# Optimization experiments

Measured on AMD Instinct MI355X. Metric: run time of the kernel, lower is better.

The kernel has to match this reference:

```python
import jax, jax.numpy as jnp
import numpy as np

E = 7       # number of experts (len(expert_details))
K = 2       # top-k routing
CAP = 3072  # per-expert capacity ~ ceil(T*K/E * 1.25)
D = 1024    # d_model
H = 4096    # d_ff = 4*d_model
T = 8192    # tokens (B=2, S=4096)


def setup_inputs() -> dict:
    key = jax.random.key(0)
    k1, k2, k3, k4 = jax.random.split(key, 4)
    x = jax.random.normal(k1, (T, D), jnp.float32)
    Wg = jax.random.normal(k2, (D, E), jnp.float32) * 0.02
    W1 = jax.random.normal(k3, (E, D, H), jnp.float32) * 0.02
    W2 = jax.random.normal(k4, (E, H, D), jnp.float32) * 0.02
    return {"x": x, "Wg": Wg, "W1": W1, "W2": W2}


def reference(x, Wg, W1, W2):
    Tn, Dn = x.shape
    # --- router ---
    gates = jax.nn.softmax(x @ Wg, axis=-1)          # [T, E]
    topw, topi = jax.lax.top_k(gates, K)             # [T, K]
    topw = topw / jnp.sum(topw, axis=-1, keepdims=True)
    flat_e = topi.reshape(-1)                        # [T*K] expert ids (int)
    flat_w = topw.reshape(-1)                        # [T*K] combine weights
    # --- position within each expert (priority = token order) ---
    onehot = jax.nn.one_hot(flat_e, E, dtype=jnp.int32)           # [T*K, E]
    pos = jnp.sum(jnp.cumsum(onehot, axis=0) * onehot, axis=-1) - 1  # [T*K]
    keep = pos < CAP
    slot = jnp.where(keep, pos, CAP)  # overflow tokens go to pad slot CAP
    # --- dispatch: scatter tokens into [E, CAP, D] buffer ---
    x_rep = jnp.repeat(x, K, axis=0)                               # [T*K, D]
    buf = jnp.zeros((E, CAP + 1, Dn), x.dtype).at[flat_e, slot].set(x_rep)[:, :CAP]
    # --- grouped expert FFN (grouped GEMMs) ---
    h = jax.nn.gelu(jnp.einsum('ecd,edh->ech', buf, W1))
    y = jnp.einsum('ech,ehd->ecd', h, W2)                          # [E, CAP, D]
    # --- combine: gather back and weight ---
    y_pad = jnp.concatenate([y, jnp.zeros((E, 1, Dn), y.dtype)], axis=1)
    out_slots = y_pad[flat_e, slot] * (flat_w * keep.astype(flat_w.dtype))[:, None]
    return out_slots.reshape(Tn, K, Dn).sum(axis=1)                # [T, D]
```

## Files before the change

### kernel.cpp

```cpp
#include <hip/hip_runtime.h>
#include <stdint.h>


#define NEXP 7
#define KTOP 2
#define CAP 3072
#define DM 1024
#define HF 4096
#define TT 8192

typedef __bf16 bf16x8 __attribute__((ext_vector_type(8)));
typedef float f32x4 __attribute__((ext_vector_type(4)));

__device__ __forceinline__ unsigned short f2bf(float v) {
  union { float f; unsigned u; } a; a.f = v;
  unsigned r = a.u + 0x7FFFu + ((a.u >> 16) & 1u);
  return (unsigned short)(r >> 16);
}
__device__ __forceinline__ float bf2f(unsigned short h) {
  union { unsigned u; float f; } a; a.u = ((unsigned)h) << 16; return a.f;
}
__device__ __forceinline__ float gelu_t(float v) {
  float u = 0.7978845608028654f * (v + 0.044715f * v * v * v);
  float ex = __expf(2.0f * u);
  float th = 1.0f - 2.0f / (ex + 1.0f);
  return 0.5f * v * (1.0f + th);
}
__device__ __forceinline__ void gl2lds16(const void* g, void* l) {
  __builtin_amdgcn_global_load_lds(
      (const __attribute__((address_space(1))) unsigned int*)g,
      (__attribute__((address_space(3))) unsigned int*)l, 16, 0, 0);
}

__global__ void init_counts(int* counts) {
  if (threadIdx.x < NEXP) counts[threadIdx.x] = 0;
}

__global__ void router_kernel(const float* __restrict__ x, const float* __restrict__ Wg,
                              int* __restrict__ counts, int* __restrict__ flatE,
                              int* __restrict__ flatSlot, int* __restrict__ tokOfSlot,
                              float* __restrict__ wOfSlot) {
  int wave = threadIdx.x >> 6, lane = threadIdx.x & 63;
  int t = blockIdx.x * 4 + wave;
  double acc[NEXP];
#pragma unroll
  for (int e = 0; e < NEXP; ++e) acc[e] = 0.0;
  const float* xr = x + (long)t * DM;
  for (int j = 0; j < DM / 64; ++j) {
    int d = j * 64 + lane;
    double xv = (double)xr[d];
#pragma unroll
    for (int e = 0; e < NEXP; ++e) acc[e] += xv * (double)Wg[d * NEXP + e];
  }
#pragma unroll
  for (int e = 0; e < NEXP; ++e) {
#pragma unroll
    for (int off = 32; off > 0; off >>= 1) acc[e] += __shfl_down(acc[e], off);
  }
  if (lane == 0) {
    int i1 = 0; double l1 = acc[0];
    for (int e2 = 1; e2 < NEXP; ++e2) if (acc[e2] > l1) { l1 = acc[e2]; i1 = e2; }
    int i2 = -1; double l2 = -1e300;
    for (int e2 = 0; e2 < NEXP; ++e2) if (e2 != i1 && acc[e2] > l2) { l2 = acc[e2]; i2 = e2; }
    float w1 = (float)(1.0 / (1.0 + exp(l2 - l1)));
    float w2 = 1.0f - w1;
    int fi0 = t * 2, fi1 = t * 2 + 1;
    int p0 = atomicAdd(&counts[i1], 1);
    flatE[fi0] = i1; flatSlot[fi0] = (p0 < CAP) ? p0 : CAP;
    if (p0 < CAP) { tokOfSlot[i1 * CAP + p0] = fi0; wOfSlot[i1 * CAP + p0] = w1; }
    int p1 = atomicAdd(&counts[i2], 1);
    flatE[fi1] = i2; flatSlot[fi1] = (p1 < CAP) ? p1 : CAP;
    if (p1 < CAP) { tokOfSlot[i2 * CAP + p1] = fi1; wOfSlot[i2 * CAP + p1] = w2; }
  }
}

__global__ void transcvt(const float* __restrict__ in, unsigned short* __restrict__ out,
                         int R, int C) {
  __shared__ float tile[64][65];
  long base = (long)blockIdx.z * (long)R * (long)C;
  const float* inp = in + base;
  unsigned short* outp = out + base;
  int c0 = blockIdx.x * 64, r0 = blockIdx.y * 64;
  int lx = threadIdx.x & 63, ly = threadIdx.x >> 6;
#pragma unroll
  for (int i = 0; i < 16; ++i) {
    int r = ly + i * 4;
    tile[r][lx] = inp[(long)(r0 + r) * C + c0 + lx];
  }
  __syncthreads();
#pragma unroll
  for (int i = 0; i < 16; ++i) {
    int c = ly + i * 4;
    outp[(long)(c0 + c) * R + r0 + lx] = f2bf(tile[lx][c]);
  }
}

__global__ void scatter_x(const float* __restrict__ x, const int* __restrict__ flatE,
                          const int* __restrict__ flatSlot, unsigned short* __restrict__ xb) {
  int fi = blockIdx.x;
  int s = flatSlot[fi];
  if (s >= CAP) return;
  int e = flatE[fi];
  const float4* xr = (const float4*)(x + (long)(fi >> 1) * DM);
  float4 v = xr[threadIdx.x];
  ushort4 o; o.x = f2bf(v.x); o.y = f2bf(v.y); o.z = f2bf(v.z); o.w = f2bf(v.w);
  ((ushort4*)(xb + ((long)e * CAP + s) * DM))[threadIdx.x] = o;
}

template <int EPI>
__global__ __launch_bounds__(512, 2) void gemm256(
    const unsigned short* __restrict__ A, const unsigned short* __restrict__ Bt,
    void* __restrict__ Cout, const int* __restrict__ counts,
    const int* __restrict__ tokOfSlot, const float* __restrict__ wOfSlot,
    int LD, int klen, int N, int kspl, long aexps, long cexps) {
  __shared__ __align__(16) unsigned short sAb[2][16384];
  __shared__ __align__(16) unsigned short sBb[2][16384];
  int e = blockIdx.z / kspl, ks = blockIdx.z % kspl;
  int mcnt = counts[e]; mcnt = mcnt < CAP ? mcnt : CAP;
  int m0 = blockIdx.y * 256;
  if (m0 >= mcnt) return;
  int n0 = blockIdx.x * 256;
  long kstart = (long)ks * klen;

  const unsigned short* Ae = A + (long)e * aexps;
  const unsigned short* Be = Bt + (long)e * (long)N * LD;

  int tid = threadIdx.x;
  int lane = tid & 63, wave = tid >> 6;
  int wr = wave >> 2, wc = wave & 3;
  int lm = lane & 15, quad = lane >> 4;

  int srow = tid >> 3;
  int scol = ((lane & 7) ^ (lane >> 3)) << 3;
  const unsigned short* As = Ae + (long)(m0 + srow) * LD + kstart + scol;
  const unsigned short* Bs = Be + (long)(n0 + srow) * LD + kstart + scol;

  int abase = (wr * 128 + lm) * 64;
  int bbase = (wc * 64 + lm) * 64;
  int cx0 = (quad ^ (lm & 7)) << 3;
  int cx1 = ((quad + 4) ^ (lm & 7)) << 3;

  f32x4 acc[8][4];
#pragma unroll
  for (int i = 0; i < 8; ++i)
#pragma unroll
    for (int j = 0; j < 4; ++j) acc[i][j] = f32x4{0.f, 0.f, 0.f, 0.f};

  int NT = klen >> 6, NI = NT >> 1;

#define STA(buf, kt, half) do { \
    int _kt = (kt) < NT ? (kt) : (NT - 1); \
    gl2lds16(As + (long)_kt * 64 + (long)((half) * 2) * 64 * LD, \
             &sAb[buf][(half) * 8192 + tid * 8]); \
    gl2lds16(As + (long)_kt * 64 + (long)((half) * 2 + 1) * 64 * LD, \
             &sAb[buf][(half) * 8192 + 4096 + tid * 8]); \
  } while (0)
#define STB(buf, kt, half) do { \
    int _kt = (kt) < NT ? (kt) : (NT - 1); \
    gl2lds16(Bs + (long)_kt * 64 + (long)((half) * 2) * 64 * LD, \
             &sBb[buf][(half) * 8192 + tid * 8]); \
    gl2lds16(Bs + (long)_kt * 64 + (long)((half) * 2 + 1) * 64 * LD, \
             &sBb[buf][(half) * 8192 + 4096 + tid * 8]); \
  } while (0)

  bf16x8 bF[4][2];

#define PHASE(buf, mi0, RB, STAGE, VM) do { \
    bf16x8 a00 = *(const bf16x8*)&sAb[buf][abase + (mi0) * 1024 + cx0]; \
    bf16x8 a01 = *(const bf16x8*)&sAb[buf][abase + (mi0) * 1024 + cx1]; \
    bf16x8 a10 = *(const bf16x8*)&sAb[buf][abase + (mi0) * 1024 + 1024 + cx0]; \
    bf16x8 a11 = *(const bf16x8*)&sAb[buf][abase + (mi0) * 1024 + 1024 + cx1]; \
    if (RB) { \
      _Pragma("unroll") \
      for (int ni = 0; ni < 4; ++ni) { \
        bF[ni][0] = *(const bf16x8*)&sBb[buf][bbase + ni * 1024 + cx0]; \
        bF[ni][1] = *(const bf16x8*)&sBb[buf][bbase + ni * 1024 + cx1]; \
      } \
    } \
    STAGE; \
    __builtin_amdgcn_s_barrier(); \
    asm volatile("s_waitcnt lgkmcnt(0)" ::: "memory"); \
    __builtin_amdgcn_sched_barrier(0); \
    __builtin_amdgcn_s_setprio(1); \
    _Pragma("unroll") \
    for (int ni = 0; ni < 4; ++ni) { \
      acc[mi0][ni]     = __builtin_amdgcn_mfma_f32_16x16x32_bf16(a00, bF[ni][0], acc[mi0][ni], 0, 0, 0); \
      acc[mi0][ni]     = __builtin_amdgcn_mfma_f32_16x16x32_bf16(a01, bF[ni][1], acc[mi0][ni], 0, 0, 0); \
      acc[mi0 + 1][ni] = __builtin_amdgcn_mfma_f32_16x16x32_bf16(a10, bF[ni][0], acc[mi0 + 1][ni], 0, 0, 0); \
      acc[mi0 + 1][ni] = __builtin_amdgcn_mfma_f32_16x16x32_bf16(a11, bF[ni][1], acc[mi0 + 1][ni], 0, 0, 0); \
    } \
    __builtin_amdgcn_s_setprio(0); \
    VM; \
    __builtin_amdgcn_s_barrier(); \
  } while (0)

  STA(0, 0, 0); STA(0, 0, 1); STB(0, 0, 0); STB(0, 0, 1);
  STB(1, 1, 0); STB(1, 1, 1);
  asm volatile("s_waitcnt vmcnt(4)" ::: "memory");
  __builtin_amdgcn_s_barrier();

  for (int t = 0; t < NI; ++t) {
    int k0 = 2 * t, k1 = 2 * t + 1;
    PHASE(0, 0, 1, STA(1, k1, 0), (void)0);
    PHASE(0, 2, 0, STA(1, k1, 1), (void)0);
    PHASE(0, 4, 0, STB(0, k0 + 2, 0), (void)0);
    PHASE(0, 6, 0, STB(0, k0 + 2, 1),
          asm volatile("s_waitcnt vmcnt(4)" ::: "memory"));
    PHASE(1, 0, 1, STA(0, k0 + 2, 0), (void)0);
    PHASE(1, 2, 0, STA(0, k0 + 2, 1), (void)0);
    PHASE(1, 4, 0, STB(1, k1 + 2, 0), (void)0);
    PHASE(1, 6, 0, STB(1, k1 + 2, 1),
          asm volatile("s_waitcnt vmcnt(4)" ::: "memory"));
  }
  asm volatile("s_waitcnt vmcnt(0)" ::: "memory");
#undef PHASE
#undef STA
#undef STB

  if (EPI == 0) {
    unsigned short* Ce = (unsigned short*)Cout + (long)e * cexps;
#pragma unroll
    for (int mi = 0; mi < 8; ++mi) {
      int mb = m0 + wr * 128 + mi * 16 + quad * 4;
#pragma unroll
      for (int r = 0; r < 4; ++r) {
        int m = mb + r;
        if (m < mcnt) {
#pragma unroll
          for (int ni = 0; ni < 4; ++ni) {
            int n = n0 + wc * 64 + ni * 16 + lm;
            Ce[(long)m * N + n] = f2bf(gelu_t(acc[mi][ni][r]));
          }
        }
      }
    }
  } else {
    unsigned short* Y = (unsigned short*)Cout + (long)ks * ((long)TT * KTOP * DM);
#pragma unroll
    for (int mi = 0; mi < 8; ++mi) {
      int mb = m0 + wr * 128 + mi * 16 + quad * 4;
#pragma unroll
      for (int r = 0; r < 4; ++r) {
        int m = mb + r;
        if (m < mcnt) {
          int fi = tokOfSlot[e * CAP + m];
          float w = wOfSlot[e * CAP + m];
#pragma unroll
          for (int ni = 0; ni < 4; ++ni) {
            int n = n0 + wc * 64 + ni * 16 + lm;
            Y[(long)fi * N + n] = f2bf(w * acc[mi][ni][r]);
          }
        }
      }
    }
  }
}

template <int EPI>
__global__ __launch_bounds__(256, 2) void gemm_bt(
    const unsigned short* __restrict__ A, const unsigned short* __restrict__ Bt,
    void* __restrict__ Cout, const int* __restrict__ counts,
    const int* __restrict__ tokOfSlot, const float* __restrict__ wOfSlot,
    int K, int N, int eoff, long aexps, long cexps) {
  __shared__ unsigned short sA[128 * 32];
  __shared__ unsigned short sB[128 * 32];
  int e = eoff + blockIdx.z;
  int mcnt = counts[e]; mcnt = mcnt < CAP ? mcnt : CAP;
  int m0 = blockIdx.y * 128;
  if (m0 >= mcnt) return;
  int n0 = blockIdx.x * 128;
  const unsigned short* Ae = A + (long)blockIdx.z * aexps;
  const unsigned short* Be = Bt + (long)e * (long)N * (long)K;

  int tid = threadIdx.x;
  int lane = tid & 63, wave = tid >> 6;
  int lm = lane & 15, quad = lane >> 4;
  int wm = (wave & 1) * 64, wn = (wave >> 1) * 64;

  int ra = tid >> 2;
  int ca = (tid & 3) * 8;
  const unsigned short* Ab0 = Ae + (long)(m0 + ra) * K + ca;
  const unsigned short* Ab1 = Ae + (long)(m0 + 64 + ra) * K + ca;
  const unsigned short* Bb0 = Be + (long)(n0 + ra) * K + ca;
  const unsigned short* Bb1 = Be + (long)(n0 + 64 + ra) * K + ca;
  unsigned short* sAp0 = &sA[tid * 8];
  unsigned short* sAp1 = &sA[(tid + 256) * 8];
  unsigned short* sBp0 = &sB[tid * 8];
  unsigned short* sBp1 = &sB[(tid + 256) * 8];

  f32x4 acc[4][4];
#pragma unroll
  for (int i = 0; i < 4; ++i)
#pragma unroll
    for (int j = 0; j < 4; ++j) acc[i][j] = f32x4{0.f, 0.f, 0.f, 0.f};

  for (int k0 = 0; k0 < K; k0 += 32) {
    gl2lds16(Ab0 + k0, sAp0);
    gl2lds16(Ab1 + k0, sAp1);
    gl2lds16(Bb0 + k0, sBp0);
    gl2lds16(Bb1 + k0, sBp1);
    __syncthreads();
    bf16x8 aF[4], bFf[4];
#pragma unroll
    for (int mi = 0; mi < 4; ++mi)
      aF[mi] = *(const bf16x8*)&sA[(wm + mi * 16 + lm) * 32 + quad * 8];
#pragma unroll
    for (int ni = 0; ni < 4; ++ni)
      bFf[ni] = *(const bf16x8*)&sB[(wn + ni * 16 + lm) * 32 + quad * 8];
#pragma unroll
    for (int mi = 0; mi < 4; ++mi)
#pragma unroll
      for (int ni = 0; ni < 4; ++ni)
        acc[mi][ni] = __builtin_amdgcn_mfma_f32_16x16x32_bf16(aF[mi], bFf[ni], acc[mi][ni], 0, 0, 0);
    __syncthreads();
  }

  if (EPI == 0) {
    unsigned short* Ce = (unsigned short*)Cout + (long)blockIdx.z * cexps;
#pragma unroll
    for (int mi = 0; mi < 4; ++mi) {
      int mb = m0 + wm + mi * 16 + quad * 4;
#pragma unroll
      for (int r = 0; r < 4; ++r) {
        int m = mb + r;
        if (m < mcnt) {
#pragma unroll
          for (int ni = 0; ni < 4; ++ni) {
            int n = n0 + wn + ni * 16 + lm;
            Ce[(long)m * N + n] = f2bf(gelu_t(acc[mi][ni][r]));
          }
        }
      }
    }
  } else {
    unsigned short* Y = (unsigned short*)Cout;
#pragma unroll
    for (int mi = 0; mi < 4; ++mi) {
      int mb = m0 + wm + mi * 16 + quad * 4;
#pragma unroll
      for (int r = 0; r < 4; ++r) {
        int m = mb + r;
        if (m < mcnt) {
          int fi = tokOfSlot[e * CAP + m];
          float w = wOfSlot[e * CAP + m];
#pragma unroll
          for (int ni = 0; ni < 4; ++ni) {
            int n = n0 + wn + ni * 16 + lm;
            Y[(long)fi * N + n] = f2bf(w * acc[mi][ni][r]);
          }
        }
      }
    }
  }
}

__global__ void combine_k2(const unsigned short* __restrict__ yflat,
                           const int* __restrict__ flatSlot, float* __restrict__ out) {
  int t = blockIdx.x;
  bool k0 = flatSlot[2 * t] < CAP, k1 = flatSlot[2 * t + 1] < CAP;
  const long S = (long)TT * KTOP * DM;
  const ushort4* y00 = (const ushort4*)(yflat + (long)(2 * t) * DM);
  const ushort4* y01 = (const ushort4*)(yflat + S + (long)(2 * t) * DM);
  const ushort4* y10 = (const ushort4*)(yflat + (long)(2 * t + 1) * DM);
  const ushort4* y11 = (const ushort4*)(yflat + S + (long)(2 * t + 1) * DM);
  ushort4 a = y00[threadIdx.x], a2 = y01[threadIdx.x];
  ushort4 b = y10[threadIdx.x], b2 = y11[threadIdx.x];
  float4 r;
  r.x = (k0 ? bf2f(a.x) + bf2f(a2.x) : 0.f) + (k1 ? bf2f(b.x) + bf2f(b2.x) : 0.f);
  r.y = (k0 ? bf2f(a.y) + bf2f(a2.y) : 0.f) + (k1 ? bf2f(b.y) + bf2f(b2.y) : 0.f);
  r.z = (k0 ? bf2f(a.z) + bf2f(a2.z) : 0.f) + (k1 ? bf2f(b.z) + bf2f(b2.z) : 0.f);
  r.w = (k0 ? bf2f(a.w) + bf2f(a2.w) : 0.f) + (k1 ? bf2f(b.w) + bf2f(b2.w) : 0.f);
  ((float4*)(out + (long)t * DM))[threadIdx.x] = r;
}

__global__ void combine_k(const unsigned short* __restrict__ yflat,
                          const int* __restrict__ flatSlot, float* __restrict__ out) {
  int t = blockIdx.x;
  bool k0 = flatSlot[2 * t] < CAP, k1 = flatSlot[2 * t + 1] < CAP;
  const ushort4* y0 = (const ushort4*)(yflat + (long)(2 * t) * DM);
  const ushort4* y1 = (const ushort4*)(yflat + (long)(2 * t + 1) * DM);
  ushort4 a = y0[threadIdx.x], b = y1[threadIdx.x];
  float4 r;
  r.x = (k0 ? bf2f(a.x) : 0.f) + (k1 ? bf2f(b.x) : 0.f);
  r.y = (k0 ? bf2f(a.y) : 0.f) + (k1 ? bf2f(b.y) : 0.f);
  r.z = (k0 ? bf2f(a.z) : 0.f) + (k1 ? bf2f(b.z) : 0.f);
  r.w = (k0 ? bf2f(a.w) : 0.f) + (k1 ? bf2f(b.w) : 0.f);
  ((float4*)(out + (long)t * DM))[threadIdx.x] = r;
}

extern "C" void kernel_launch(void* const* d_in, const int* in_sizes, int n_in,
                              void* d_out, int out_size, void* d_ws, size_t ws_size,
                              hipStream_t stream) {
  const float* x  = (const float*)d_in[0];
  const float* Wg = (const float*)d_in[1];
  const float* W1 = (const float*)d_in[2];
  const float* W2 = (const float*)d_in[3];
  float* out = (float*)d_out;

  char* ws = (char*)d_ws;
  size_t off = 0;
  auto alloc = [&](size_t b) { void* p = ws + off; off = (off + b + 255) & ~(size_t)255; return p; };
  int* counts            = (int*)alloc(NEXP * 4);
  int* flatE             = (int*)alloc((size_t)TT * KTOP * 4);
  int* flatSlot          = (int*)alloc((size_t)TT * KTOP * 4);
  int* tokOfSlot         = (int*)alloc((size_t)NEXP * CAP * 4);
  float* wOfSlot         = (float*)alloc((size_t)NEXP * CAP * 4);
  unsigned short* Wb1    = (unsigned short*)alloc((size_t)NEXP * DM * HF * 2);
  unsigned short* Wb2    = (unsigned short*)alloc((size_t)NEXP * DM * HF * 2);
  unsigned short* xb     = (unsigned short*)alloc((size_t)NEXP * CAP * DM * 2);
  unsigned short* yflat  = (unsigned short*)alloc((size_t)2 * TT * KTOP * DM * 2);
  size_t hbA = (size_t)NEXP * CAP * HF * 2;
  size_t hbB = (size_t)CAP * HF * 2;
  int planA = (off + hbA) <= ws_size;
  unsigned short* hb = (unsigned short*)alloc(planA ? hbA : hbB);

  init_counts<<<1, 64, 0, stream>>>(counts);
  router_kernel<<<TT / 4, 256, 0, stream>>>(x, Wg, counts, flatE, flatSlot, tokOfSlot, wOfSlot);
  transcvt<<<dim3(HF / 64, DM / 64, NEXP), 256, 0, stream>>>(W1, Wb1, DM, HF);
  transcvt<<<dim3(DM / 64, HF / 64, NEXP), 256, 0, stream>>>(W2, Wb2, HF, DM);
  scatter_x<<<TT * KTOP, 256, 0, stream>>>(x, flatE, flatSlot, xb);

  if (planA) {
    gemm256<0><<<dim3(HF / 256, CAP / 256, NEXP), 512, 0, stream>>>(
        xb, Wb1, hb, counts, tokOfSlot, wOfSlot, DM, DM, HF, 1,
        (long)CAP * DM, (long)CAP * HF);
    gemm256<1><<<dim3(DM / 256, CAP / 256, NEXP * 2), 512, 0, stream>>>(
        hb, Wb2, yflat, counts, tokOfSlot, wOfSlot, HF, HF / 2, DM, 2,
        (long)CAP * HF, 0);
    combine_k2<<<TT, 256, 0, stream>>>(yflat, flatSlot, out);
  } else {
    for (int e = 0; e < NEXP; ++e) {
      gemm_bt<0><<<dim3(HF / 128, CAP / 128, 1), 256, 0, stream>>>(
          xb + (size_t)e * CAP * DM, Wb1, hb, counts, tokOfSlot, wOfSlot, DM, HF, e, 0, 0);
      gemm_bt<1><<<dim3(DM / 128, CAP / 128, 1), 256, 0, stream>>>(
          hb, Wb2, yflat, counts, tokOfSlot, wOfSlot, HF, DM, e, 0, 0);
    }
    combine_k<<<TT, 256, 0, stream>>>(yflat, flatSlot, out);
  }
}
```

Baseline: 930.7 us.

## Shrink grouped-GEMM tile to 256x128 with 4x2 wave layout and new pipeline

Changes the block tile of the expert GEMMs from 256x256 to 256x128, rearranging 8 waves as 4 rows by 2 columns and halving per-thread accumulators. The load/compute pipeline is rewritten into two phases per k-step, with A rows staged in interleaved quarters and B tile loads reduced accordingly. The aim is more blocks for better CU coverage and lower register/LDS pressure, at the cost of lower arithmetic intensity and more global traffic per FLOP.

Measured after the change: 1.017 ms. 1.09x slower.

```diff
diff --git a/kernel.cpp b/kernel.cpp
--- a/kernel.cpp
+++ b/kernel.cpp
@@ -113,13 +113,14 @@
     void* __restrict__ Cout, const int* __restrict__ counts,
     const int* __restrict__ tokOfSlot, const float* __restrict__ wOfSlot,
     int LD, int klen, int N, int kspl, long aexps, long cexps) {
-  __shared__ __align__(16) unsigned short sAb[2][16384];
-  __shared__ __align__(16) unsigned short sBb[2][16384];
+  __shared__ __align__(16) unsigned short sA[2][16384];
+  __shared__ __align__(16) unsigned short sB[2][8192];
+
   int e = blockIdx.z / kspl, ks = blockIdx.z % kspl;
   int mcnt = counts[e]; mcnt = mcnt < CAP ? mcnt : CAP;
   int m0 = blockIdx.y * 256;
   if (m0 >= mcnt) return;
-  int n0 = blockIdx.x * 256;
+  int n0 = blockIdx.x * 128;
   long kstart = (long)ks * klen;
 
   const unsigned short* Ae = A + (long)e * aexps;
@@ -127,101 +128,119 @@
 
   int tid = threadIdx.x;
   int lane = tid & 63, wave = tid >> 6;
-  int wr = wave >> 2, wc = wave & 3;
+  int wr = wave >> 1, wc = wave & 1;
   int lm = lane & 15, quad = lane >> 4;
 
-  int srow = tid >> 3;
+  int u8 = tid >> 3;
   int scol = ((lane & 7) ^ (lane >> 3)) << 3;
-  const unsigned short* As = Ae + (long)(m0 + srow) * LD + kstart + scol;
-  const unsigned short* Bs = Be + (long)(n0 + srow) * LD + kstart + scol;
-
-  int abase = (wr * 128 + lm) * 64;
+  int wb0 = ((u8 >> 5) & 3) * 64 + (u8 & 31);
+  int wb1 = ((2 + (u8 >> 5)) & 3) * 64 + (u8 & 31);
+  const unsigned short* As0 = Ae + (long)(m0 + wb0) * LD + kstart + scol;
+  const unsigned short* As1 = Ae + (long)(m0 + wb1) * LD + kstart + scol;
+  const unsigned short* As2 = Ae + (long)(m0 + wb0 + 32) * LD + kstart + scol;
+  const unsigned short* As3 = Ae + (long)(m0 + wb1 + 32) * LD + kstart + scol;
+  const unsigned short* Bs0 = Be + (long)(n0 + u8) * LD + kstart + scol;
+  const unsigned short* Bs1 = Be + (long)(n0 + 64 + u8) * LD + kstart + scol;
+
+  int aslo = (wr * 32 + lm) * 64;
+  int ashi = aslo + 8192;
   int bbase = (wc * 64 + lm) * 64;
   int cx0 = (quad ^ (lm & 7)) << 3;
   int cx1 = ((quad + 4) ^ (lm & 7)) << 3;
 
-  f32x4 acc[8][4];
-#pragma unroll
-  for (int i = 0; i < 8; ++i)
+  f32x4 acc[4][4];
+#pragma unroll
+  for (int i = 0; i < 4; ++i)
 #pragma unroll
     for (int j = 0; j < 4; ++j) acc[i][j] = f32x4{0.f, 0.f, 0.f, 0.f};
 
-  int NT = klen >> 6, NI = NT >> 1;
-
-#define STA(buf, kt, half) do { \
-    int _kt = (kt) < NT ? (kt) : (NT - 1); \
-    gl2lds16(As + (long)_kt * 64 + (long)((half) * 2) * 64 * LD, \
-             &sAb[buf][(half) * 8192 + tid * 8]); \
-    gl2lds16(As + (long)_kt * 64 + (long)((half) * 2 + 1) * 64 * LD, \
-             &sAb[buf][(half) * 8192 + 4096 + tid * 8]); \
-  } while (0)
-#define STB(buf, kt, half) do { \
-    int _kt = (kt) < NT ? (kt) : (NT - 1); \
-    gl2lds16(Bs + (long)_kt * 64 + (long)((half) * 2) * 64 * LD, \
-             &sBb[buf][(half) * 8192 + tid * 8]); \
-    gl2lds16(Bs + (long)_kt * 64 + (long)((half) * 2 + 1) * 64 * LD, \
-             &sBb[buf][(half) * 8192 + 4096 + tid * 8]); \
-  } while (0)
+  int NT = klen >> 6;
+
+#define CLMP(t) ((t) < NT ? (t) : (NT - 1))
+#define SA_(b, kt, i) gl2lds16(As##i + (long)CLMP(kt) * 64, &sA[b][(i) * 4096 + tid * 8])
+#define SB_(b, kt, i) gl2lds16(Bs##i + (long)CLMP(kt) * 64, &sB[b][(i) * 4096 + tid * 8])
+
+#define MFMA_(a, b, c) __builtin_amdgcn_mfma_f32_16x16x32_bf16(a, b, c, 0, 0, 0)
 
   bf16x8 bF[4][2];
 
-#define PHASE(buf, mi0, RB, STAGE, VM) do { \
-    bf16x8 a00 = *(const bf16x8*)&sAb[buf][abase + (mi0) * 1024 + cx0]; \
-    bf16x8 a01 = *(const bf16x8*)&sAb[buf][abase + (mi0) * 1024 + cx1]; \
-    bf16x8 a10 = *(const bf16x8*)&sAb[buf][abase + (mi0) * 1024 + 1024 + cx0]; \
-    bf16x8 a11 = *(const bf16x8*)&sAb[buf][abase + (mi0) * 1024 + 1024 + cx1]; \
-    if (RB) { \
-      _Pragma("unroll") \
-      for (int ni = 0; ni < 4; ++ni) { \
-        bF[ni][0] = *(const bf16x8*)&sBb[buf][bbase + ni * 1024 + cx0]; \
-        bF[ni][1] = *(const bf16x8*)&sBb[buf][bbase + ni * 1024 + cx1]; \
-      } \
-    } \
-    STAGE; \
+#define PH1(B, STG) do { \
+    bf16x8 a00 = *(const bf16x8*)&sA[B][aslo + cx0]; \
+    bf16x8 a01 = *(const bf16x8*)&sA[B][aslo + cx1]; \
+    bf16x8 a10 = *(const bf16x8*)&sA[B][aslo + 1024 + cx0]; \
+    bf16x8 a11 = *(const bf16x8*)&sA[B][aslo + 1024 + cx1]; \
+    bF[0][0] = *(const bf16x8*)&sB[B][bbase + cx0]; \
+    bF[0][1] = *(const bf16x8*)&sB[B][bbase + cx1]; \
+    bF[1][0] = *(const bf16x8*)&sB[B][bbase + 1024 + cx0]; \
+    bF[1][1] = *(const bf16x8*)&sB[B][bbase + 1024 + cx1]; \
+    bF[2][0] = *(const bf16x8*)&sB[B][bbase + 2048 + cx0]; \
+    bF[2][1] = *(const bf16x8*)&sB[B][bbase + 2048 + cx1]; \
+    bF[3][0] = *(const bf16x8*)&sB[B][bbase + 3072 + cx0]; \
+    bF[3][1] = *(const bf16x8*)&sB[B][bbase + 3072 + cx1]; \
+    STG; \
     __builtin_amdgcn_s_barrier(); \
     asm volatile("s_waitcnt lgkmcnt(0)" ::: "memory"); \
     __builtin_amdgcn_sched_barrier(0); \
     __builtin_amdgcn_s_setprio(1); \
-    _Pragma("unroll") \
-    for (int ni = 0; ni < 4; ++ni) { \
-      acc[mi0][ni]     = __builtin_amdgcn_mfma_f32_16x16x32_bf16(a00, bF[ni][0], acc[mi0][ni], 0, 0, 0); \
-      acc[mi0][ni]     = __builtin_amdgcn_mfma_f32_16x16x32_bf16(a01, bF[ni][1], acc[mi0][ni], 0, 0, 0); \
-      acc[mi0 + 1][ni] = __builtin_amdgcn_mfma_f32_16x16x32_bf16(a10, bF[ni][0], acc[mi0 + 1][ni], 0, 0, 0); \
-      acc[mi0 + 1][ni] = __builtin_amdgcn_mfma_f32_16x16x32_bf16(a11, bF[ni][1], acc[mi0 + 1][ni], 0, 0, 0); \
-    } \
+    acc[0][0] = MFMA_(a00, bF[0][0], acc[0][0]); acc[0][0] = MFMA_(a01, bF[0][1], acc[0][0]); \
+    acc[0][1] = MFMA_(a00, bF[1][0], acc[0][1]); acc[0][1] = MFMA_(a01, bF[1][1], acc[0][1]); \
+    acc[0][2] = MFMA_(a00, bF[2][0], acc[0][2]); acc[0][2] = MFMA_(a01, bF[2][1], acc[0][2]); \
+    acc[0][3] = MFMA_(a00, bF[3][0], acc[0][3]); acc[0][3] = MFMA_(a01, bF[3][1], acc[0][3]); \
+    acc[1][0] = MFMA_(a10, bF[0][0], acc[1][0]); acc[1][0] = MFMA_(a11, bF[0][1], acc[1][0]); \
+    acc[1][1] = MFMA_(a10, bF[1][0], acc[1][1]); acc[1][1] = MFMA_(a11, bF[1][1], acc[1][1]); \
+    acc[1][2] = MFMA_(a10, bF[2][0], acc[1][2]); acc[1][2] = MFMA_(a11, bF[2][1], acc[1][2]); \
+    acc[1][3] = MFMA_(a10, bF[3][0], acc[1][3]); acc[1][3] = MFMA_(a11, bF[3][1], acc[1][3]); \
     __builtin_amdgcn_s_setprio(0); \
-    VM; \
     __builtin_amdgcn_s_barrier(); \
   } while (0)
 
-  STA(0, 0, 0); STA(0, 0, 1); STB(0, 0, 0); STB(0, 0, 1);
-  STB(1, 1, 0); STB(1, 1, 1);
+#define PH2(B, STG) do { \
+    bf16x8 a20 = *(const bf16x8*)&sA[B][ashi + cx0]; \
+    bf16x8 a21 = *(const bf16x8*)&sA[B][ashi + cx1]; \
+    bf16x8 a30 = *(const bf16x8*)&sA[B][ashi + 1024 + cx0]; \
+    bf16x8 a31 = *(const bf16x8*)&sA[B][ashi + 1024 + cx1]; \
+    STG; \
+    __builtin_amdgcn_s_barrier(); \
+    asm volatile("s_waitcnt lgkmcnt(0)" ::: "memory"); \
+    __builtin_amdgcn_sched_barrier(0); \
+    __builtin_amdgcn_s_setprio(1); \
+    acc[2][0] = MFMA_(a20, bF[0][0], acc[2][0]); acc[2][0] = MFMA_(a21, bF[0][1], acc[2][0]); \
+    acc[2][1] = MFMA_(a20, bF[1][0], acc[2][1]); acc[2][1] = MFMA_(a21, bF[1][1], acc[2][1]); \
+    acc[2][2] = MFMA_(a20, bF[2][0], acc[2][2]); acc[2][2] = MFMA_(a21, bF[2][1], acc[2][2]); \
+    acc[2][3] = MFMA_(a20, bF[3][0], acc[2][3]); acc[2][3] = MFMA_(a21, bF[3][1], acc[2][3]); \
+    acc[3][0] = MFMA_(a30, bF[0][0], acc[3][0]); acc[3][0] = MFMA_(a31, bF[0][1], acc[3][0]); \
+    acc[3][1] = MFMA_(a30, bF[1][0], acc[3][1]); acc[3][1] = MFMA_(a31, bF[1][1], acc[3][1]); \
+    acc[3][2] = MFMA_(a30, bF[2][0], acc[3][2]); acc[3][2] = MFMA_(a31, bF[2][1], acc[3][2]); \
+    acc[3][3] = MFMA_(a30, bF[3][0], acc[3][3]); acc[3][3] = MFMA_(a31, bF[3][1], acc[3][3]); \
+    __builtin_amdgcn_s_setprio(0); \
+    asm volatile("s_waitcnt vmcnt(4)" ::: "memory"); \
+    __builtin_amdgcn_s_barrier(); \
+  } while (0)
+
+  SA_(0, 0, 0); SA_(0, 0, 1); SA_(0, 0, 2); SA_(0, 0, 3); SB_(0, 0, 0); SB_(0, 0, 1);
+  SB_(1, 1, 0); SB_(1, 1, 1); SA_(1, 1, 0); SA_(1, 1, 1);
   asm volatile("s_waitcnt vmcnt(4)" ::: "memory");
   __builtin_amdgcn_s_barrier();
 
-  for (int t = 0; t < NI; ++t) {
-    int k0 = 2 * t, k1 = 2 * t + 1;
-    PHASE(0, 0, 1, STA(1, k1, 0), (void)0);
-    PHASE(0, 2, 0, STA(1, k1, 1), (void)0);
-    PHASE(0, 4, 0, STB(0, k0 + 2, 0), (void)0);
-    PHASE(0, 6, 0, STB(0, k0 + 2, 1),
-          asm volatile("s_waitcnt vmcnt(4)" ::: "memory"));
-    PHASE(1, 0, 1, STA(0, k0 + 2, 0), (void)0);
-    PHASE(1, 2, 0, STA(0, k0 + 2, 1), (void)0);
-    PHASE(1, 4, 0, STB(1, k1 + 2, 0), (void)0);
-    PHASE(1, 6, 0, STB(1, k1 + 2, 1),
-          asm volatile("s_waitcnt vmcnt(4)" ::: "memory"));
+  for (int t = 0; t < NT; t += 2) {
+    PH1(0, { SA_(1, t + 1, 2); SA_(1, t + 1, 3); });
+    PH2(0, { SB_(0, t + 2, 0); SB_(0, t + 2, 1); SA_(0, t + 2, 0); SA_(0, t + 2, 1); });
+    PH1(1, { SA_(0, t + 2, 2); SA_(0, t + 2, 3); });
+    PH2(1, { SB_(1, t + 3, 0); SB_(1, t + 3, 1); SA_(1, t + 3, 0); SA_(1, t + 3, 1); });
   }
   asm volatile("s_waitcnt vmcnt(0)" ::: "memory");
-#undef PHASE
-#undef STA
-#undef STB
+#undef PH1
+#undef PH2
+#undef MFMA_
+#undef SA_
+#undef SB_
+#undef CLMP
 
   if (EPI == 0) {
     unsigned short* Ce = (unsigned short*)Cout + (long)e * cexps;
 #pragma unroll
-    for (int mi = 0; mi < 8; ++mi) {
-      int mb = m0 + wr * 128 + mi * 16 + quad * 4;
+    for (int mi = 0; mi < 4; ++mi) {
+      int mb = m0 + wr * 64 + mi * 16 + quad * 4;
 #pragma unroll
       for (int r = 0; r < 4; ++r) {
         int m = mb + r;
@@ -237,18 +256,18 @@
   } else {
     unsigned short* Y = (unsigned short*)Cout + (long)ks * ((long)TT * KTOP * DM);
 #pragma unroll
-    for (int mi = 0; mi < 8; ++mi) {
-      int mb = m0 + wr * 128 + mi * 16 + quad * 4;
+    for (int mi = 0; mi < 4; ++mi) {
+      int mb = m0 + wr * 64 + mi * 16 + quad * 4;
 #pragma unroll
       for (int r = 0; r < 4; ++r) {
         int m = mb + r;
         if (m < mcnt) {
           int fi = tokOfSlot[e * CAP + m];
-          float w = wOfSlot[e * CAP + m];
+          float wgt = wOfSlot[e * CAP + m];
 #pragma unroll
           for (int ni = 0; ni < 4; ++ni) {
             int n = n0 + wc * 64 + ni * 16 + lm;
-            Y[(long)fi * N + n] = f2bf(w * acc[mi][ni][r]);
+            Y[(long)fi * N + n] = f2bf(wgt * acc[mi][ni][r]);
           }
         }
       }
@@ -421,10 +440,10 @@
   scatter_x<<<TT * KTOP, 256, 0, stream>>>(x, flatE, flatSlot, xb);
 
   if (planA) {
-    gemm256<0><<<dim3(HF / 256, CAP / 256, NEXP), 512, 0, stream>>>(
+    gemm256<0><<<dim3(HF / 128, CAP / 256, NEXP), 512, 0, stream>>>(
         xb, Wb1, hb, counts, tokOfSlot, wOfSlot, DM, DM, HF, 1,
         (long)CAP * DM, (long)CAP * HF);
-    gemm256<1><<<dim3(DM / 256, CAP / 256, NEXP * 2), 512, 0, stream>>>(
+    gemm256<1><<<dim3(DM / 128, CAP / 256, NEXP * 2), 512, 0, stream>>>(
         hb, Wb2, yflat, counts, tokOfSlot, wOfSlot, HF, HF / 2, DM, 2,
         (long)CAP * HF, 0);
     combine_k2<<<TT, 256, 0, stream>>>(yflat, flatSlot, out);
```

## Fuse router and token scatter into one kernel with block-local slot allocation

Applied to the files above, without the earlier changes.

Replaces the per-token router and the separate scatter_x kernel with a single kernel that handles 32 tokens per block. Wg is staged transposed in shared memory, x is read as float4, and each block builds a local expert histogram so it needs one global atomic per expert instead of one per token. The same kernel then converts and writes the bf16 rows into the expert buffers, which removes a launch and the flatE round trip. Slot order within an expert now depends on the order of block atomics rather than token order, which can change which tokens overflow when an expert exceeds capacity.

Measured after the change: 782.6 us. 1.19x faster.

```diff
diff --git a/kernel.cpp b/kernel.cpp
--- a/kernel.cpp
+++ b/kernel.cpp
@@ -8,6 +8,7 @@
 #define DM 1024
 #define HF 4096
 #define TT 8192
+#define RBLK 32
 
 typedef __bf16 bf16x8 __attribute__((ext_vector_type(8)));
 typedef float f32x4 __attribute__((ext_vector_type(4)));
@@ -36,41 +37,88 @@
   if (threadIdx.x < NEXP) counts[threadIdx.x] = 0;
 }
 
-__global__ void router_kernel(const float* __restrict__ x, const float* __restrict__ Wg,
-                              int* __restrict__ counts, int* __restrict__ flatE,
-                              int* __restrict__ flatSlot, int* __restrict__ tokOfSlot,
-                              float* __restrict__ wOfSlot) {
-  int wave = threadIdx.x >> 6, lane = threadIdx.x & 63;
-  int t = blockIdx.x * 4 + wave;
-  double acc[NEXP];
-#pragma unroll
-  for (int e = 0; e < NEXP; ++e) acc[e] = 0.0;
-  const float* xr = x + (long)t * DM;
-  for (int j = 0; j < DM / 64; ++j) {
-    int d = j * 64 + lane;
-    double xv = (double)xr[d];
-#pragma unroll
-    for (int e = 0; e < NEXP; ++e) acc[e] += xv * (double)Wg[d * NEXP + e];
-  }
-#pragma unroll
-  for (int e = 0; e < NEXP; ++e) {
-#pragma unroll
-    for (int off = 32; off > 0; off >>= 1) acc[e] += __shfl_down(acc[e], off);
-  }
-  if (lane == 0) {
-    int i1 = 0; double l1 = acc[0];
-    for (int e2 = 1; e2 < NEXP; ++e2) if (acc[e2] > l1) { l1 = acc[e2]; i1 = e2; }
-    int i2 = -1; double l2 = -1e300;
-    for (int e2 = 0; e2 < NEXP; ++e2) if (e2 != i1 && acc[e2] > l2) { l2 = acc[e2]; i2 = e2; }
-    float w1 = (float)(1.0 / (1.0 + exp(l2 - l1)));
-    float w2 = 1.0f - w1;
-    int fi0 = t * 2, fi1 = t * 2 + 1;
-    int p0 = atomicAdd(&counts[i1], 1);
-    flatE[fi0] = i1; flatSlot[fi0] = (p0 < CAP) ? p0 : CAP;
-    if (p0 < CAP) { tokOfSlot[i1 * CAP + p0] = fi0; wOfSlot[i1 * CAP + p0] = w1; }
-    int p1 = atomicAdd(&counts[i2], 1);
-    flatE[fi1] = i2; flatSlot[fi1] = (p1 < CAP) ? p1 : CAP;
-    if (p1 < CAP) { tokOfSlot[i2 * CAP + p1] = fi1; wOfSlot[i2 * CAP + p1] = w2; }
+__global__ __launch_bounds__(256) void router_fused(
+    const float* __restrict__ x, const float* __restrict__ Wg,
+    int* __restrict__ counts, int* __restrict__ flatSlot,
+    int* __restrict__ tokOfSlot, float* __restrict__ wOfSlot,
+    unsigned short* __restrict__ xb) {
+  __shared__ float sWgT[NEXP][DM];
+  __shared__ int hist[NEXP], base[NEXP];
+  __shared__ int pickE[RBLK * 2];
+  __shared__ int pickR[RBLK * 2];
+  __shared__ float pickW[RBLK * 2];
+  int tid = threadIdx.x, lane = tid & 63, wave = tid >> 6;
+
+  for (int i = tid; i < NEXP * DM; i += 256) {
+    int e = i / DM, d = i - e * DM;
+    sWgT[e][d] = Wg[d * NEXP + e];
+  }
+  if (tid < NEXP) hist[tid] = 0;
+  __syncthreads();
+
+  for (int tt = wave; tt < RBLK; tt += 4) {
+    int t = blockIdx.x * RBLK + tt;
+    const float4* xr = (const float4*)(x + (long)t * DM);
+    double acc[NEXP];
+#pragma unroll
+    for (int e = 0; e < NEXP; ++e) acc[e] = 0.0;
+#pragma unroll
+    for (int j = 0; j < 4; ++j) {
+      float4 xv = xr[j * 64 + lane];
+      int d4 = (j * 64 + lane) * 4;
+#pragma unroll
+      for (int e = 0; e < NEXP; ++e) {
+        float4 wv = *(const float4*)&sWgT[e][d4];
+        acc[e] += (double)xv.x * (double)wv.x + (double)xv.y * (double)wv.y
+                + (double)xv.z * (double)wv.z + (double)xv.w * (double)wv.w;
+      }
+    }
+#pragma unroll
+    for (int e = 0; e < NEXP; ++e) {
+#pragma unroll
+      for (int off = 32; off > 0; off >>= 1) acc[e] += __shfl_down(acc[e], off);
+    }
+    if (lane == 0) {
+      int i1 = 0; double l1 = acc[0];
+      for (int e2 = 1; e2 < NEXP; ++e2) if (acc[e2] > l1) { l1 = acc[e2]; i1 = e2; }
+      int i2 = -1; double l2 = -1e300;
+      for (int e2 = 0; e2 < NEXP; ++e2) if (e2 != i1 && acc[e2] > l2) { l2 = acc[e2]; i2 = e2; }
+      float w1 = (float)(1.0 / (1.0 + exp(l2 - l1)));
+      int r0 = atomicAdd(&hist[i1], 1);
+      int r1 = atomicAdd(&hist[i2], 1);
+      pickE[2 * tt] = i1;     pickR[2 * tt] = r0;     pickW[2 * tt] = w1;
+      pickE[2 * tt + 1] = i2; pickR[2 * tt + 1] = r1; pickW[2 * tt + 1] = 1.0f - w1;
+    }
+  }
+  __syncthreads();
+  if (tid < NEXP) base[tid] = atomicAdd(&counts[tid], hist[tid]);
+  __syncthreads();
+
+  for (int tt = wave; tt < RBLK; tt += 4) {
+    int t = blockIdx.x * RBLK + tt;
+    const float4* xr = (const float4*)(x + (long)t * DM);
+    float4 v0 = xr[0 * 64 + lane], v1 = xr[1 * 64 + lane];
+    float4 v2 = xr[2 * 64 + lane], v3 = xr[3 * 64 + lane];
+    ushort4 o0, o1, o2, o3;
+    o0.x = f2bf(v0.x); o0.y = f2bf(v0.y); o0.z = f2bf(v0.z); o0.w = f2bf(v0.w);
+    o1.x = f2bf(v1.x); o1.y = f2bf(v1.y); o1.z = f2bf(v1.z); o1.w = f2bf(v1.w);
+    o2.x = f2bf(v2.x); o2.y = f2bf(v2.y); o2.z = f2bf(v2.z); o2.w = f2bf(v2.w);
+    o3.x = f2bf(v3.x); o3.y = f2bf(v3.y); o3.z = f2bf(v3.z); o3.w = f2bf(v3.w);
+#pragma unroll
+    for (int p = 0; p < 2; ++p) {
+      int e = pickE[2 * tt + p];
+      int s = base[e] + pickR[2 * tt + p];
+      int fi = t * 2 + p;
+      if (lane == 0) {
+        flatSlot[fi] = (s < CAP) ? s : CAP;
+        if (s < CAP) { tokOfSlot[e * CAP + s] = fi; wOfSlot[e * CAP + s] = pickW[2 * tt + p]; }
+      }
+      if (s < CAP) {
+        ushort4* dst = (ushort4*)(xb + ((long)e * CAP + s) * DM);
+        dst[0 * 64 + lane] = o0; dst[1 * 64 + lane] = o1;
+        dst[2 * 64 + lane] = o2; dst[3 * 64 + lane] = o3;
+      }
+    }
   }
 }
 
@@ -93,18 +141,6 @@
     int c = ly + i * 4;
     outp[(long)(c0 + c) * R + r0 + lx] = f2bf(tile[lx][c]);
   }
-}
-
-__global__ void scatter_x(const float* __restrict__ x, const int* __restrict__ flatE,
-                          const int* __restrict__ flatSlot, unsigned short* __restrict__ xb) {
-  int fi = blockIdx.x;
-  int s = flatSlot[fi];
-  if (s >= CAP) return;
-  int e = flatE[fi];
-  const float4* xr = (const float4*)(x + (long)(fi >> 1) * DM);
-  float4 v = xr[threadIdx.x];
-  ushort4 o; o.x = f2bf(v.x); o.y = f2bf(v.y); o.z = f2bf(v.z); o.w = f2bf(v.w);
-  ((ushort4*)(xb + ((long)e * CAP + s) * DM))[threadIdx.x] = o;
 }
 
 template <int EPI>
@@ -401,7 +437,6 @@
   size_t off = 0;
   auto alloc = [&](size_t b) { void* p = ws + off; off = (off + b + 255) & ~(size_t)255; return p; };
   int* counts            = (int*)alloc(NEXP * 4);
-  int* flatE             = (int*)alloc((size_t)TT * KTOP * 4);
   int* flatSlot          = (int*)alloc((size_t)TT * KTOP * 4);
   int* tokOfSlot         = (int*)alloc((size_t)NEXP * CAP * 4);
   float* wOfSlot         = (float*)alloc((size_t)NEXP * CAP * 4);
@@ -415,10 +450,9 @@
   unsigned short* hb = (unsigned short*)alloc(planA ? hbA : hbB);
 
   init_counts<<<1, 64, 0, stream>>>(counts);
-  router_kernel<<<TT / 4, 256, 0, stream>>>(x, Wg, counts, flatE, flatSlot, tokOfSlot, wOfSlot);
+  router_fused<<<TT / RBLK, 256, 0, stream>>>(x, Wg, counts, flatSlot, tokOfSlot, wOfSlot, xb);
   transcvt<<<dim3(HF / 64, DM / 64, NEXP), 256, 0, stream>>>(W1, Wb1, DM, HF);
   transcvt<<<dim3(DM / 64, HF / 64, NEXP), 256, 0, stream>>>(W2, Wb2, HF, DM);
-  scatter_x<<<TT * KTOP, 256, 0, stream>>>(x, flatE, flatSlot, xb);
 
   if (planA) {
     gemm256<0><<<dim3(HF / 256, CAP / 256, NEXP), 512, 0, stream>>>(
```
